# Kernel tuning notes

Hardware: AMD Instinct MI355X
Metric: run time of the kernel (lower is better)

The kernel has to match this reference:

```python
import jax, jax.numpy as jnp
import numpy as np

N_NODES = 50000   # r_mat is [N_NODES, N_NODES] sparse
N_REL = 1000      # number of relations (rows of dual_layer)
D = 128           # node / relation feature dim
NNZ = 800000      # number of edges (nnz of r_mat)


def setup_inputs() -> dict:
    key = jax.random.key(0)
    k1, k2, k3, k4, k5, k6 = jax.random.split(key, 6)
    return {
        "inlayer": jax.random.normal(k1, (N_NODES, D), jnp.float32),
        "dual_layer": jax.random.normal(k2, (N_REL, D), jnp.float32),
        # Conv1d(in=D, out=1, kernel=1): weight [1, D, 1] -> vector [D], bias [1]
        "conv_w": jax.random.normal(k3, (D,), jnp.float32) * (1.0 / np.sqrt(D)),
        "conv_b": jax.random.normal(k4, (1,), jnp.float32) * 0.01,
        # COO indices of r_mat: row = destination node, col = source node
        "edge_idx": jax.random.randint(k5, (2, NNZ), 0, N_NODES, dtype=jnp.int32),
        # r_mat._values(): integer relation id per edge
        "edge_rel": jax.random.randint(k6, (NNZ,), 0, N_REL, dtype=jnp.int32),
    }


def reference(inlayer, dual_layer, conv_w, conv_b, edge_idx, edge_rel):
    # conv1d with kernel_size=1 over [1, D, n_rel] == per-relation linear -> [n_rel]
    scores = dual_layer @ conv_w + conv_b[0]
    # gather per-edge logit by relation id
    logits = scores[edge_rel]                                  # [nnz]
    # NOTE: original applies leaky_relu then softmax GLOBALLY over all nnz edges
    coefs = jax.nn.softmax(jax.nn.leaky_relu(logits))          # [nnz]
    row, col = edge_idx[0], edge_idx[1]
    # sparse-dense matmul: out[r] = sum_{e: row[e]=r} coefs[e] * inlayer[col[e]]
    out = jax.ops.segment_sum(coefs[:, None] * inlayer[col], row,
                              num_segments=N_NODES)            # [N, D]
    # act_func=None path of the original forward
    return out
```

## Files before the change

kernel.cpp:

```cpp
#include <hip/hip_runtime.h>
#include <hip/hip_fp16.h>
#include <math.h>

#define N_NODES 50000
#define N_REL   1000
#define D       128
#define NNZ     800000

#define RB    512
#define NBIN  98
#define CAP   10240
#define CH    1024
#define NCH   ((NNZ + CH - 1) / CH)
#define K1T   256
#define K1E   (CH / K1T)
#define PBT   512

__global__ void __launch_bounds__(K1T)
k1_kernel(const int* __restrict__ rows, const int* __restrict__ cols,
          const int* __restrict__ rel, const float* __restrict__ dual,
          const float* __restrict__ conv_w, const float* __restrict__ conv_b,
          const float* __restrict__ inlayer, float* __restrict__ exp_scores,
          unsigned* __restrict__ bincur, unsigned long long* __restrict__ binbuf,
          __half2* __restrict__ hinl) {
    __shared__ unsigned long long sbuf[CH];
    __shared__ unsigned char sbin[CH];
    __shared__ unsigned lcnt[NBIN], lstart[NBIN], lgb[NBIN];
    __shared__ unsigned w0sum;
    int t = threadIdx.x;
    int gtid = blockIdx.x * K1T + t;
    int lane = t & 63;

    int wid = gtid >> 6;
    if (wid < N_REL) {
        const float* row = dual + (long)wid * D;
        float s = row[lane] * conv_w[lane] + row[lane + 64] * conv_w[lane + 64];
        #pragma unroll
        for (int off = 32; off > 0; off >>= 1) s += __shfl_down(s, off);
        if (lane == 0) {
            float v = s + conv_b[0];
            v = (v >= 0.f) ? v : 0.01f * v;
            exp_scores[wid] = expf(v);
        }
    }

    const float4* src4 = (const float4*)inlayer;
    uint2* dst2 = (uint2*)hinl;
    for (int i = gtid; i < N_NODES * D / 4; i += NCH * K1T) {
        float4 f = src4[i];
        __half2 h0 = __floats2half2_rn(f.x, f.y);
        __half2 h1 = __floats2half2_rn(f.z, f.w);
        uint2 o; o.x = *(unsigned*)&h0; o.y = *(unsigned*)&h1;
        dst2[i] = o;
    }

    for (int i = t; i < NBIN; i += K1T) lcnt[i] = 0;
    __syncthreads();

    int base = blockIdx.x * CH;
    int n = NNZ - base; if (n > CH) n = CH;

    int       ebin[K1E];
    unsigned  erank[K1E];
    unsigned long long epack[K1E];
    #pragma unroll
    for (int k = 0; k < K1E; ++k) {
        int j = k * K1T + t;
        if (j < n) {
            int e = base + j;
            int r = rows[e], c = cols[e], q = rel[e];
            int b = r >> 9;
            epack[k] = (unsigned long long)(unsigned)c
                     | ((unsigned long long)(unsigned)q << 16)
                     | ((unsigned long long)(unsigned)(r & 511) << 26);
            ebin[k] = b;
            erank[k] = atomicAdd(&lcnt[b], 1u);
        } else ebin[k] = -1;
    }
    __syncthreads();

    unsigned v = (t < NBIN) ? lcnt[t] : 0u;
    if (t < 128) {
        #pragma unroll
        for (int off = 1; off < 64; off <<= 1) {
            unsigned y = __shfl_up(v, off);
            if (lane >= off) v += y;
        }
        if (t == 63) w0sum = v;
    }
    __syncthreads();
    if (t >= 64 && t < 128) v += w0sum;
    if (t < NBIN) {
        lstart[t] = v - lcnt[t];
        lgb[t] = atomicAdd(&bincur[t * 16], lcnt[t]);
    }
    __syncthreads();

    #pragma unroll
    for (int k = 0; k < K1E; ++k) {
        if (ebin[k] >= 0) {
            unsigned p = lstart[ebin[k]] + erank[k];
            sbuf[p] = epack[k];
            sbin[p] = (unsigned char)ebin[k];
        }
    }
    __syncthreads();

    #pragma unroll
    for (int k = 0; k < K1E; ++k) {
        int j = k * K1T + t;
        if (j < n) {
            int b = sbin[j];
            unsigned slot = lgb[b] + (unsigned)j - lstart[b];
            if (slot < CAP)
                binbuf[(unsigned long long)b * CAP + slot] = sbuf[j];
        }
    }
}

__global__ void __launch_bounds__(PBT)
place_kernel(const unsigned* __restrict__ bincur,
             const unsigned long long* __restrict__ binbuf,
             const float* __restrict__ exp_scores,
             unsigned* __restrict__ starts, unsigned* __restrict__ bpack,
             float* __restrict__ denom) {
    __shared__ unsigned cnt[RB], cur[RB], ex[RB];
    __shared__ unsigned wsum[8];
    __shared__ float    rpart[8];
    __shared__ unsigned sh_binbase;
    int t = threadIdx.x, lane = t & 63, w = t >> 6;
    int b = blockIdx.x;
    int rlo = b * RB;
    unsigned nb = bincur[b * 16]; if (nb > CAP) nb = CAP;
    const unsigned long long* bb = binbuf + (unsigned long long)b * CAP;

    cnt[t] = 0; cur[t] = 0;
    __syncthreads();
    for (int e = t; e < (int)nb; e += PBT) {
        unsigned long long pk = bb[e];
        atomicAdd(&cnt[(pk >> 26) & 511ULL], 1u);
    }
    __syncthreads();

    {
        unsigned bv = (t < b) ? min(bincur[t * 16], (unsigned)CAP) : 0u;
        #pragma unroll
        for (int off = 32; off > 0; off >>= 1) bv += __shfl_down(bv, off);
        if (lane == 0) wsum[w] = bv;
        __syncthreads();
        if (t == 0) {
            unsigned s = 0;
            #pragma unroll
            for (int k = 0; k < 8; ++k) s += wsum[k];
            sh_binbase = s;
        }
        __syncthreads();
    }

    unsigned c0 = cnt[t];
    unsigned v = c0;
    #pragma unroll
    for (int off = 1; off < 64; off <<= 1) {
        unsigned y = __shfl_up(v, off);
        if (lane >= off) v += y;
    }
    if (lane == 63) wsum[w] = v;
    __syncthreads();
    if (t == 0) {
        unsigned acc = 0;
        #pragma unroll
        for (int k = 0; k < 8; ++k) { unsigned tmp = wsum[k]; wsum[k] = acc; acc += tmp; }
    }
    __syncthreads();
    unsigned gex = sh_binbase + wsum[w] + (v - c0);
    ex[t] = gex;
    if (rlo + t <= N_NODES) starts[rlo + t] = gex;
    __syncthreads();

    float dsum = 0.f;
    for (int e = t; e < (int)nb; e += PBT) {
        unsigned long long pk = bb[e];
        int r = (int)((pk >> 26) & 511ULL);
        unsigned lp = (unsigned)(pk & 0x3FFFFFFULL);
        unsigned rank = atomicAdd(&cur[r], 1u);
        bpack[ex[r] + rank] = lp;
        dsum += exp_scores[lp >> 16];
    }
    #pragma unroll
    for (int off = 32; off > 0; off >>= 1) dsum += __shfl_down(dsum, off);
    if (lane == 0) rpart[w] = dsum;
    __syncthreads();
    if (t == 0) {
        float s = 0.f;
        #pragma unroll
        for (int k = 0; k < 8; ++k) s += rpart[k];
        atomicAdd(denom, s);
    }
}

__global__ void gather_kernel(const unsigned* __restrict__ starts,
                              const unsigned* __restrict__ bpack,
                              const float* __restrict__ exp_scores,
                              const __half2* __restrict__ hinl,
                              const float* __restrict__ denom,
                              float* __restrict__ out) {
    int node = blockIdx.x * (blockDim.x >> 6) + (threadIdx.x >> 6);
    int lane = threadIdx.x & 63;
    if (node >= N_NODES) return;
    int s = (int)starts[node];
    int e = (int)starts[node + 1];
    int quad = lane >> 4;
    int l16  = lane & 15;
    float a0=0.f,a1=0.f,a2=0.f,a3=0.f,a4=0.f,a5=0.f,a6=0.f,a7=0.f;
    for (int base = s; base < e; base += 64) {
        int rem = e - base; if (rem > 64) rem = 64;
        int px = 0, py = 0;
        if (lane < rem) {
            unsigned pk = bpack[base + lane];
            px = (int)(pk & 0xFFFFu);
            py = __float_as_int(exp_scores[pk >> 16]);
        }
        for (int j = 0; j < rem; j += 16) {
            #pragma unroll
            for (int k = 0; k < 16; k += 4) {
                if (j + k < rem) {
                    int idx = j + k + quad;
                    int   c = __shfl(px, idx);
                    float wv = __int_as_float(__shfl(py, idx));
                    const __half2* hp = hinl + (long)c * (D / 2) + l16 * 4;
                    uint4 hv = *(const uint4*)hp;
                    float2 f0 = __half22float2(*(const __half2*)&hv.x);
                    float2 f1 = __half22float2(*(const __half2*)&hv.y);
                    float2 f2 = __half22float2(*(const __half2*)&hv.z);
                    float2 f3 = __half22float2(*(const __half2*)&hv.w);
                    a0 += wv * f0.x; a1 += wv * f0.y;
                    a2 += wv * f1.x; a3 += wv * f1.y;
                    a4 += wv * f2.x; a5 += wv * f2.y;
                    a6 += wv * f3.x; a7 += wv * f3.y;
                }
            }
        }
    }
    #define COMB(x) x += __shfl(x, lane ^ 16); x += __shfl(x, lane ^ 32);
    COMB(a0) COMB(a1) COMB(a2) COMB(a3) COMB(a4) COMB(a5) COMB(a6) COMB(a7)
    #undef COMB
    if (lane < 32) {
        float inv = 1.0f / *denom;
        float4 v;
        int hi = (lane >> 4) & 1;
        if (hi) { v.x = a4*inv; v.y = a5*inv; v.z = a6*inv; v.w = a7*inv; }
        else    { v.x = a0*inv; v.y = a1*inv; v.z = a2*inv; v.w = a3*inv; }
        *(float4*)(out + (long)node * D + l16 * 8 + hi * 4) = v;
    }
}

extern "C" void kernel_launch(void* const* d_in, const int* in_sizes, int n_in,
                              void* d_out, int out_size, void* d_ws, size_t ws_size,
                              hipStream_t stream) {
    const float* inlayer  = (const float*)d_in[0];
    const float* dual     = (const float*)d_in[1];
    const float* conv_w   = (const float*)d_in[2];
    const float* conv_b   = (const float*)d_in[3];
    const int*   edge_idx = (const int*)d_in[4];
    const int*   edge_rel = (const int*)d_in[5];
    float* out = (float*)d_out;
    const int* rows = edge_idx;
    const int* cols = edge_idx + NNZ;

    char* ws = (char*)d_ws;
    float*              exp_scores = (float*)             (ws);
    float*              denom      = (float*)             (ws + 4096);
    unsigned*           bincur     = (unsigned*)          (ws + 8192);
    unsigned*           starts     = (unsigned*)          (ws + 16384);
    unsigned long long* binbuf     = (unsigned long long*)(ws + 221184);
    unsigned*           bpack      = (unsigned*)          (ws + 8249344);
    __half2*            hinl       = (__half2*)           (ws + 11449344);

    hipMemsetAsync(ws + 4096, 0, 4096 + 98 * 16 * 4, stream);

    k1_kernel<<<NCH, K1T, 0, stream>>>(rows, cols, edge_rel, dual, conv_w, conv_b,
                                       inlayer, exp_scores, bincur, binbuf, hinl);
    place_kernel<<<NBIN, PBT, 0, stream>>>(bincur, binbuf, exp_scores,
                                           starts, bpack, denom);
    int grid = (N_NODES + 3) / 4;
    gather_kernel<<<grid, 256, 0, stream>>>(starts, bpack, exp_scores,
                                            hinl, denom, out);
}
```

Baseline: 154.4 us.

## Use finer row bins, larger edge chunks, and vectorized edge loads

Row bins shrink from 512 to 128 rows, which raises the place-kernel grid from 98 to 391 blocks and gives more parallelism in the bucketing pass. The binning kernel now takes 2048 edges per block with 512 threads and reads rows, cols and rel as int4 vectors. The place kernel keeps its packed edges in registers between the count and scatter passes, so binbuf is read once instead of twice. Risks are a more complex per-block prefix scan and higher per-bin overflow risk with the smaller CAP of 2560 entries.

```diff
diff --git a/kernel.cpp b/kernel.cpp
--- a/kernel.cpp
+++ b/kernel.cpp
@@ -7,14 +7,15 @@
 #define D       128
 #define NNZ     800000
 
-#define RB    512
-#define NBIN  98
-#define CAP   10240
-#define CH    1024
+#define RB    128
+#define NBIN  391
+#define CAP   2560
+#define CH    2048
 #define NCH   ((NNZ + CH - 1) / CH)
-#define K1T   256
+#define K1T   512
 #define K1E   (CH / K1T)
 #define PBT   512
+#define PE    (CAP / PBT)
 
 __global__ void __launch_bounds__(K1T)
 k1_kernel(const int* __restrict__ rows, const int* __restrict__ cols,
@@ -24,12 +25,12 @@
           unsigned* __restrict__ bincur, unsigned long long* __restrict__ binbuf,
           __half2* __restrict__ hinl) {
     __shared__ unsigned long long sbuf[CH];
-    __shared__ unsigned char sbin[CH];
+    __shared__ unsigned short sbin[CH];
     __shared__ unsigned lcnt[NBIN], lstart[NBIN], lgb[NBIN];
-    __shared__ unsigned w0sum;
+    __shared__ unsigned wsum[8];
     int t = threadIdx.x;
     int gtid = blockIdx.x * K1T + t;
-    int lane = t & 63;
+    int lane = t & 63, w = t >> 6;
 
     int wid = gtid >> 6;
     if (wid < N_REL) {
@@ -59,40 +60,52 @@
 
     int base = blockIdx.x * CH;
     int n = NNZ - base; if (n > CH) n = CH;
+    int base4 = blockIdx.x * (CH / 4);
 
     int       ebin[K1E];
     unsigned  erank[K1E];
     unsigned long long epack[K1E];
+    bool has = (4 * t < n);
+    int4 rr, cc, qq;
+    if (has) {
+        rr = ((const int4*)rows)[base4 + t];
+        cc = ((const int4*)cols)[base4 + t];
+        qq = ((const int4*)rel)[base4 + t];
+    }
     #pragma unroll
     for (int k = 0; k < K1E; ++k) {
-        int j = k * K1T + t;
-        if (j < n) {
-            int e = base + j;
-            int r = rows[e], c = cols[e], q = rel[e];
-            int b = r >> 9;
+        if (has) {
+            int r = (k == 0) ? rr.x : (k == 1) ? rr.y : (k == 2) ? rr.z : rr.w;
+            int c = (k == 0) ? cc.x : (k == 1) ? cc.y : (k == 2) ? cc.z : cc.w;
+            int q = (k == 0) ? qq.x : (k == 1) ? qq.y : (k == 2) ? qq.z : qq.w;
+            int b = r >> 7;
             epack[k] = (unsigned long long)(unsigned)c
                      | ((unsigned long long)(unsigned)q << 16)
-                     | ((unsigned long long)(unsigned)(r & 511) << 26);
+                     | ((unsigned long long)(unsigned)(r & 127) << 26);
             ebin[k] = b;
             erank[k] = atomicAdd(&lcnt[b], 1u);
         } else ebin[k] = -1;
     }
     __syncthreads();
 
-    unsigned v = (t < NBIN) ? lcnt[t] : 0u;
-    if (t < 128) {
-        #pragma unroll
-        for (int off = 1; off < 64; off <<= 1) {
-            unsigned y = __shfl_up(v, off);
-            if (lane >= off) v += y;
-        }
-        if (t == 63) w0sum = v;
-    }
-    __syncthreads();
-    if (t >= 64 && t < 128) v += w0sum;
+    unsigned cb = (t < NBIN) ? lcnt[t] : 0u;
+    unsigned v = cb;
+    #pragma unroll
+    for (int off = 1; off < 64; off <<= 1) {
+        unsigned y = __shfl_up(v, off);
+        if (lane >= off) v += y;
+    }
+    if (lane == 63) wsum[w] = v;
+    __syncthreads();
+    if (t == 0) {
+        unsigned acc = 0;
+        #pragma unroll
+        for (int k = 0; k < 8; ++k) { unsigned tmp = wsum[k]; wsum[k] = acc; acc += tmp; }
+    }
+    __syncthreads();
     if (t < NBIN) {
-        lstart[t] = v - lcnt[t];
-        lgb[t] = atomicAdd(&bincur[t * 16], lcnt[t]);
+        lstart[t] = wsum[w] + (v - cb);
+        lgb[t] = atomicAdd(&bincur[t * 16], cb);
     }
     __syncthreads();
 
@@ -101,7 +114,7 @@
         if (ebin[k] >= 0) {
             unsigned p = lstart[ebin[k]] + erank[k];
             sbuf[p] = epack[k];
-            sbin[p] = (unsigned char)ebin[k];
+            sbin[p] = (unsigned short)ebin[k];
         }
     }
     __syncthreads();
@@ -134,30 +147,34 @@
     unsigned nb = bincur[b * 16]; if (nb > CAP) nb = CAP;
     const unsigned long long* bb = binbuf + (unsigned long long)b * CAP;
 
-    cnt[t] = 0; cur[t] = 0;
-    __syncthreads();
-    for (int e = t; e < (int)nb; e += PBT) {
-        unsigned long long pk = bb[e];
-        atomicAdd(&cnt[(pk >> 26) & 511ULL], 1u);
-    }
-    __syncthreads();
-
-    {
-        unsigned bv = (t < b) ? min(bincur[t * 16], (unsigned)CAP) : 0u;
-        #pragma unroll
-        for (int off = 32; off > 0; off >>= 1) bv += __shfl_down(bv, off);
-        if (lane == 0) wsum[w] = bv;
-        __syncthreads();
-        if (t == 0) {
-            unsigned s = 0;
-            #pragma unroll
-            for (int k = 0; k < 8; ++k) s += wsum[k];
-            sh_binbase = s;
-        }
-        __syncthreads();
-    }
-
-    unsigned c0 = cnt[t];
+    if (t < RB) { cnt[t] = 0; cur[t] = 0; }
+    __syncthreads();
+
+    unsigned long long epk[PE];
+    #pragma unroll
+    for (int k = 0; k < PE; ++k) {
+        int e = t + k * PBT;
+        if (e < (int)nb) {
+            unsigned long long pk = bb[e];
+            epk[k] = pk;
+            atomicAdd(&cnt[(pk >> 26) & 127ULL], 1u);
+        }
+    }
+
+    unsigned bv = (t < b) ? min(bincur[t * 16], (unsigned)CAP) : 0u;
+    #pragma unroll
+    for (int off = 32; off > 0; off >>= 1) bv += __shfl_down(bv, off);
+    if (lane == 0) wsum[w] = bv;
+    __syncthreads();
+    if (t == 0) {
+        unsigned s = 0;
+        #pragma unroll
+        for (int k = 0; k < 8; ++k) s += wsum[k];
+        sh_binbase = s;
+    }
+    __syncthreads();
+
+    unsigned c0 = (t < RB) ? cnt[t] : 0u;
     unsigned v = c0;
     #pragma unroll
     for (int off = 1; off < 64; off <<= 1) {
@@ -173,18 +190,23 @@
     }
     __syncthreads();
     unsigned gex = sh_binbase + wsum[w] + (v - c0);
-    ex[t] = gex;
-    if (rlo + t <= N_NODES) starts[rlo + t] = gex;
+    if (t < RB) ex[t] = gex;
+    if (t <= RB && rlo + t <= N_NODES)
+        starts[rlo + t] = gex;
     __syncthreads();
 
     float dsum = 0.f;
-    for (int e = t; e < (int)nb; e += PBT) {
-        unsigned long long pk = bb[e];
-        int r = (int)((pk >> 26) & 511ULL);
-        unsigned lp = (unsigned)(pk & 0x3FFFFFFULL);
-        unsigned rank = atomicAdd(&cur[r], 1u);
-        bpack[ex[r] + rank] = lp;
-        dsum += exp_scores[lp >> 16];
+    #pragma unroll
+    for (int k = 0; k < PE; ++k) {
+        int e = t + k * PBT;
+        if (e < (int)nb) {
+            unsigned long long pk = epk[k];
+            int r = (int)((pk >> 26) & 127ULL);
+            unsigned lp = (unsigned)(pk & 0x3FFFFFFULL);
+            unsigned rank = atomicAdd(&cur[r], 1u);
+            bpack[ex[r] + rank] = lp;
+            dsum += exp_scores[lp >> 16];
+        }
     }
     #pragma unroll
     for (int off = 32; off > 0; off >>= 1) dsum += __shfl_down(dsum, off);
@@ -271,12 +293,12 @@
     float*              exp_scores = (float*)             (ws);
     float*              denom      = (float*)             (ws + 4096);
     unsigned*           bincur     = (unsigned*)          (ws + 8192);
-    unsigned*           starts     = (unsigned*)          (ws + 16384);
-    unsigned long long* binbuf     = (unsigned long long*)(ws + 221184);
-    unsigned*           bpack      = (unsigned*)          (ws + 8249344);
-    __half2*            hinl       = (__half2*)           (ws + 11449344);
-
-    hipMemsetAsync(ws + 4096, 0, 4096 + 98 * 16 * 4, stream);
+    unsigned*           starts     = (unsigned*)          (ws + 36864);
+    unsigned long long* binbuf     = (unsigned long long*)(ws + 245760);
+    unsigned*           bpack      = (unsigned*)          (ws + 245760 + 8007680);
+    __half2*            hinl       = (__half2*)           (ws + 245760 + 8007680 + 3200000);
+
+    hipMemsetAsync(ws + 4096, 0, 4096 + NBIN * 64, stream);
 
     k1_kernel<<<NCH, K1T, 0, stream>>>(rows, cols, edge_rel, dual, conv_w, conv_b,
                                        inlayer, exp_scores, bincur, binbuf, hinl);
```

New measurement: 143.3 us. -7.2%, faster.

## Split place kernel into per-bin sub-blocks and vectorize edge loads in k1

Applied to the files above, without the earlier changes.

The place kernel now launches four blocks per row bin, each owning 128 rows instead of 512. Each block rescans the whole bin, counts only its own rows, and derives its output base from the count of lower sub-bin edges. This raises the grid from 98 blocks to 392 so more CUs are busy, at the cost of reading each bin four times. The k1 kernel doubles its chunk size and thread count, and each thread now loads four consecutive edges with int4 vector loads instead of strided scalar loads.

```diff
diff --git a/kernel.cpp b/kernel.cpp
--- a/kernel.cpp
+++ b/kernel.cpp
@@ -10,9 +10,10 @@
 #define RB    512
 #define NBIN  98
 #define CAP   10240
-#define CH    1024
+#define SUBR  128
+#define CH    2048
 #define NCH   ((NNZ + CH - 1) / CH)
-#define K1T   256
+#define K1T   512
 #define K1E   (CH / K1T)
 #define PBT   512
 
@@ -54,21 +55,28 @@
         dst2[i] = o;
     }
 
-    for (int i = t; i < NBIN; i += K1T) lcnt[i] = 0;
-    __syncthreads();
-
-    int base = blockIdx.x * CH;
-    int n = NNZ - base; if (n > CH) n = CH;
+    if (t < NBIN) lcnt[t] = 0;
+    __syncthreads();
+
+    int n = NNZ - blockIdx.x * CH; if (n > CH) n = CH;
+    int base4 = blockIdx.x * (CH / 4);
 
     int       ebin[K1E];
     unsigned  erank[K1E];
     unsigned long long epack[K1E];
+    bool has = (4 * t < n);
+    int4 rr, cc, qq;
+    if (has) {
+        rr = ((const int4*)rows)[base4 + t];
+        cc = ((const int4*)cols)[base4 + t];
+        qq = ((const int4*)rel)[base4 + t];
+    }
     #pragma unroll
     for (int k = 0; k < K1E; ++k) {
-        int j = k * K1T + t;
-        if (j < n) {
-            int e = base + j;
-            int r = rows[e], c = cols[e], q = rel[e];
+        if (has) {
+            int r = (k == 0) ? rr.x : (k == 1) ? rr.y : (k == 2) ? rr.z : rr.w;
+            int c = (k == 0) ? cc.x : (k == 1) ? cc.y : (k == 2) ? cc.z : cc.w;
+            int q = (k == 0) ? qq.x : (k == 1) ? qq.y : (k == 2) ? qq.z : qq.w;
             int b = r >> 9;
             epack[k] = (unsigned long long)(unsigned)c
                      | ((unsigned long long)(unsigned)q << 16)
@@ -124,40 +132,45 @@
              const float* __restrict__ exp_scores,
              unsigned* __restrict__ starts, unsigned* __restrict__ bpack,
              float* __restrict__ denom) {
-    __shared__ unsigned cnt[RB], cur[RB], ex[RB];
-    __shared__ unsigned wsum[8];
+    __shared__ unsigned cnt[SUBR], cur[SUBR], ex[SUBR];
+    __shared__ unsigned wsum[8], bsum[8];
     __shared__ float    rpart[8];
-    __shared__ unsigned sh_binbase;
+    __shared__ unsigned sh_base;
     int t = threadIdx.x, lane = t & 63, w = t >> 6;
-    int b = blockIdx.x;
-    int rlo = b * RB;
+    int b   = blockIdx.x >> 2;
+    int sub = blockIdx.x & 3;
+    int rlo = b * RB + sub * SUBR;
     unsigned nb = bincur[b * 16]; if (nb > CAP) nb = CAP;
     const unsigned long long* bb = binbuf + (unsigned long long)b * CAP;
 
-    cnt[t] = 0; cur[t] = 0;
-    __syncthreads();
+    if (t < SUBR) { cnt[t] = 0; cur[t] = 0; }
+    __syncthreads();
+
+    unsigned below = 0;
     for (int e = t; e < (int)nb; e += PBT) {
-        unsigned long long pk = bb[e];
-        atomicAdd(&cnt[(pk >> 26) & 511ULL], 1u);
-    }
-    __syncthreads();
-
-    {
-        unsigned bv = (t < b) ? min(bincur[t * 16], (unsigned)CAP) : 0u;
-        #pragma unroll
-        for (int off = 32; off > 0; off >>= 1) bv += __shfl_down(bv, off);
-        if (lane == 0) wsum[w] = bv;
-        __syncthreads();
-        if (t == 0) {
-            unsigned s = 0;
-            #pragma unroll
-            for (int k = 0; k < 8; ++k) s += wsum[k];
-            sh_binbase = s;
-        }
-        __syncthreads();
-    }
-
-    unsigned c0 = cnt[t];
+        unsigned u = (unsigned)(bb[e] >> 26);
+        unsigned us = u >> 7;
+        if (us == (unsigned)sub) atomicAdd(&cnt[u & 127], 1u);
+        below += (us < (unsigned)sub) ? 1u : 0u;
+    }
+
+    unsigned bv = (t < b) ? min(bincur[t * 16], (unsigned)CAP) : 0u;
+    #pragma unroll
+    for (int off = 32; off > 0; off >>= 1) {
+        bv    += __shfl_down(bv, off);
+        below += __shfl_down(below, off);
+    }
+    if (lane == 0) { wsum[w] = bv; bsum[w] = below; }
+    __syncthreads();
+    if (t == 0) {
+        unsigned s = 0;
+        #pragma unroll
+        for (int k = 0; k < 8; ++k) s += wsum[k] + bsum[k];
+        sh_base = s;
+    }
+    __syncthreads();
+
+    unsigned c0 = (t < SUBR) ? cnt[t] : 0u;
     unsigned v = c0;
     #pragma unroll
     for (int off = 1; off < 64; off <<= 1) {
@@ -172,19 +185,23 @@
         for (int k = 0; k < 8; ++k) { unsigned tmp = wsum[k]; wsum[k] = acc; acc += tmp; }
     }
     __syncthreads();
-    unsigned gex = sh_binbase + wsum[w] + (v - c0);
-    ex[t] = gex;
-    if (rlo + t <= N_NODES) starts[rlo + t] = gex;
+    unsigned base = sh_base;
+    if (t < SUBR) ex[t] = wsum[w] + (v - c0);
+    if (t < SUBR && rlo + t <= N_NODES)
+        starts[rlo + t] = base + wsum[w] + (v - c0);
     __syncthreads();
 
     float dsum = 0.f;
     for (int e = t; e < (int)nb; e += PBT) {
         unsigned long long pk = bb[e];
-        int r = (int)((pk >> 26) & 511ULL);
-        unsigned lp = (unsigned)(pk & 0x3FFFFFFULL);
-        unsigned rank = atomicAdd(&cur[r], 1u);
-        bpack[ex[r] + rank] = lp;
-        dsum += exp_scores[lp >> 16];
+        unsigned u = (unsigned)(pk >> 26);
+        if ((u >> 7) == (unsigned)sub) {
+            int r = (int)(u & 127);
+            unsigned rank = atomicAdd(&cur[r], 1u);
+            unsigned lp = (unsigned)(pk & 0x3FFFFFFULL);
+            bpack[base + ex[r] + rank] = lp;
+            dsum += exp_scores[lp >> 16];
+        }
     }
     #pragma unroll
     for (int off = 32; off > 0; off >>= 1) dsum += __shfl_down(dsum, off);
@@ -272,16 +289,16 @@
     float*              denom      = (float*)             (ws + 4096);
     unsigned*           bincur     = (unsigned*)          (ws + 8192);
     unsigned*           starts     = (unsigned*)          (ws + 16384);
-    unsigned long long* binbuf     = (unsigned long long*)(ws + 221184);
-    unsigned*           bpack      = (unsigned*)          (ws + 8249344);
-    __half2*            hinl       = (__half2*)           (ws + 11449344);
-
-    hipMemsetAsync(ws + 4096, 0, 4096 + 98 * 16 * 4, stream);
+    unsigned long long* binbuf     = (unsigned long long*)(ws + 217088);
+    unsigned*           bpack      = (unsigned*)          (ws + 8245248);
+    __half2*            hinl       = (__half2*)           (ws + 11445248);
+
+    hipMemsetAsync(ws + 4096, 0, 4096 + NBIN * 64, stream);
 
     k1_kernel<<<NCH, K1T, 0, stream>>>(rows, cols, edge_rel, dual, conv_w, conv_b,
                                        inlayer, exp_scores, bincur, binbuf, hinl);
-    place_kernel<<<NBIN, PBT, 0, stream>>>(bincur, binbuf, exp_scores,
-                                           starts, bpack, denom);
+    place_kernel<<<NBIN * 4, PBT, 0, stream>>>(bincur, binbuf, exp_scores,
+                                               starts, bpack, denom);
     int grid = (N_NODES + 3) / 4;
     gather_kernel<<<grid, 256, 0, stream>>>(starts, bpack, exp_scores,
                                             hinl, denom, out);
```

Measured after the change: 148.8 us. -3.7%, faster.
